# Performance work log

Measured on AMD Instinct MI355X. Metric: run time of the kernel, lower is better.

## Reference

```python
import jax, jax.numpy as jnp
import numpy as np

C = 5.0          # tanh clamp constant (args.c, non-trainable)
B, N, R, D = 4, 16, 64, 256  # batch, block_num, block_len, word_dim
NEG = -1e9


def setup_inputs() -> dict:
    key = jax.random.key(0)
    ks = iter(jax.random.split(key, 80))

    def W(i, o):
        # xavier-like init (torch stores (out,in); we store (in,out) and use x @ W)
        return jax.random.normal(next(ks), (i, o), jnp.float32) * np.float32(np.sqrt(2.0 / (i + o)))

    def bvec(d):
        return jax.random.normal(next(ks), (d,), jnp.float32) * 0.01

    inp = {"x": jax.random.normal(next(ks), (B, N, R, D), jnp.float32)}
    for p in ("fw", "bw"):
        inp[f"fcW_{p}"] = W(D, D);  inp[f"fcb_{p}"] = bvec(D)
        inp[f"mW1_{p}"] = W(D, D);  inp[f"mW2_{p}"] = W(D, D);  inp[f"mb_{p}"] = bvec(D)
        inp[f"s2tW1_{p}"] = W(D, D); inp[f"s2tb1_{p}"] = bvec(D)
        inp[f"s2tW_{p}"] = W(D, D);  inp[f"s2tb_{p}"] = bvec(D)
        inp[f"gW1_{p}"] = W(D, D);  inp[f"gW2_{p}"] = W(D, D);  inp[f"gb_{p}"] = bvec(D)
        inp[f"fW1_{p}"] = W(3 * D, D); inp[f"fb1_{p}"] = bvec(D)
        inp[f"fW2_{p}"] = W(3 * D, D); inp[f"fb2_{p}"] = bvec(D)
    return inp


def _mSA(x, W1, W2, b, fw):
    # x: (..., L, d) -> (..., L, d). Additive per-feature attention with strict
    # triangular mask. fw: token i attends to j > i (last row zeroed);
    # bw: token i attends to j < i (first row zeroed). Matches the torch
    # -inf mask + narrow + zero-pad construction exactly.
    L = x.shape[-2]
    xi = (x @ W1)[..., :, None, :]                 # (..., L, 1, d)
    xj = (x @ W2)[..., None, :, :]                 # (..., 1, L, d)
    f = C * jnp.tanh((xi + xj + b) / C)            # (..., i, j, d)
    i = jnp.arange(L)[:, None]
    j = jnp.arange(L)[None, :]
    allowed = (j > i) if fw else (j < i)           # (L, L)
    scores = jnp.where(allowed[..., None], f, NEG)
    att = jax.nn.softmax(scores, axis=-2)          # softmax over j
    rowvalid = (jnp.arange(L) < L - 1) if fw else (jnp.arange(L) > 0)
    att = att * rowvalid[:, None, None].astype(x.dtype)
    return jnp.einsum('...ijd,...jd->...id', att, x)


def _s2t(x, W1, b1, Wo, bo):
    # source2token self-attention: (..., L, d) -> (..., d)
    f = jax.nn.relu(x @ W1 + b1)
    a = jax.nn.softmax(f @ Wo + bo, axis=-2)
    return jnp.sum(a * x, axis=-2)


def _mblosa(x, mW1, mW2, mb, s2tW1, s2tb1, s2tW, s2tb,
            gW1, gW2, gb, fW1, fb1, fW2, fb2, fw):
    Bb, n, r, d = x.shape
    h = _mSA(x, mW1, mW2, mb, fw)                  # (B, n, r, d) intra-block
    v = _s2t(h, s2tW1, s2tb1, s2tW, s2tb)          # (B, n, d)    block summary
    o = _mSA(v, mW1, mW2, mb, fw)                  # (B, n, d)    inter-block
    G = jax.nn.sigmoid(o @ gW1 + v @ gW2 + gb)
    e = G * o + (1.0 - G) * v                      # (B, n, d)
    # torch: cat of e[i] repeated r times, then narrow(1, 0, n)
    idx = jnp.arange(n) // r
    E = e[:, idx]                                  # (B, n, d)
    # torch: flatten blocks then narrow(1, 0, n) (faithful to source)
    xf = x.reshape(Bb, n * r, d)[:, :n]
    hf = h.reshape(Bb, n * r, d)[:, :n]
    cat = jnp.concatenate([xf, hf, E], axis=-1)    # (B, n, 3d)
    fusion = jax.nn.relu(cat @ fW1 + fb1)
    Gf = jax.nn.sigmoid(cat @ fW2 + fb2)
    return Gf * fusion + (1.0 - Gf) * xf           # (B, n, d)


def reference(x,
              fcW_fw, fcb_fw, mW1_fw, mW2_fw, mb_fw, s2tW1_fw, s2tb1_fw,
              s2tW_fw, s2tb_fw, gW1_fw, gW2_fw, gb_fw, fW1_fw, fb1_fw,
              fW2_fw, fb2_fw,
              fcW_bw, fcb_bw, mW1_bw, mW2_bw, mb_bw, s2tW1_bw, s2tb1_bw,
              s2tW_bw, s2tb_bw, gW1_bw, gW2_bw, gb_bw, fW1_bw, fb1_bw,
              fW2_bw, fb2_bw):
    in_fw = jax.nn.relu(x @ fcW_fw + fcb_fw)
    in_bw = jax.nn.relu(x @ fcW_bw + fcb_bw)
    u_fw = _mblosa(in_fw, mW1_fw, mW2_fw, mb_fw, s2tW1_fw, s2tb1_fw,
                   s2tW_fw, s2tb_fw, gW1_fw, gW2_fw, gb_fw,
                   fW1_fw, fb1_fw, fW2_fw, fb2_fw, True)
    u_bw = _mblosa(in_bw, mW1_bw, mW2_bw, mb_bw, s2tW1_bw, s2tb1_bw,
                   s2tW_bw, s2tb_bw, gW1_bw, gW2_bw, gb_bw,
                   fW1_bw, fb1_bw, fW2_bw, fb2_bw, False)
    return jnp.concatenate([u_fw, u_bw], axis=-1)  # (B, n, 2d)
```

## Files before the change

### kernel.cpp

```cpp
#include <hip/hip_runtime.h>
#include <hip/hip_bf16.h>

typedef __hip_bfloat16 BF16;
typedef __attribute__((ext_vector_type(8))) short short8;
typedef __attribute__((ext_vector_type(4))) float f32x4;

#define MFMA_B16(a,b,c) __builtin_amdgcn_mfma_f32_16x16x32_bf16((a),(b),(c),0,0,0)

__device__ __forceinline__ short f2bs(float f){ BF16 h = __float2bfloat16(f); return *(short*)&h; }
__device__ __forceinline__ float bs2f(short s){ BF16 h = *(BF16*)&s; return __bfloat162float(h); }

struct SrcPack { const float* s[10]; };

__global__ __launch_bounds__(256) void transpose_k(SrcPack p, short* __restrict__ Oh,
                                                   short* __restrict__ Ol)
{
    __shared__ float s[64][65];
    const float* W = p.s[blockIdx.y];
    short* oh = Oh + (size_t)blockIdx.y * 65536;
    short* ol = Ol + (size_t)blockIdx.y * 65536;
    int tr = (blockIdx.x >> 2) * 64, tc = (blockIdx.x & 3) * 64;
    #pragma unroll
    for (int i = 0; i < 16; i++) {
        int e = threadIdx.x + i * 256;
        int r = e >> 6, c = e & 63;
        s[c][r] = W[(size_t)(tr + r) * 256 + tc + c];
    }
    __syncthreads();
    #pragma unroll
    for (int i = 0; i < 16; i++) {
        int e = threadIdx.x + i * 256;
        int c2 = e >> 6, r2 = e & 63;
        float v = s[c2][r2];
        short hi = f2bs(v);
        short lo = f2bs(v - bs2f(hi));
        size_t oi = (size_t)(tc + c2) * 256 + tr + r2;
        oh[oi] = hi;
        ol[oi] = lo;
    }
}

template<int AM, int OM, int RELU, int BS>
__device__ __forceinline__ void gemm_body(const void* __restrict__ A0,
    const void* __restrict__ Alo,
    const short* __restrict__ Wh, const short* __restrict__ Wl,
    const float* __restrict__ bias, void* __restrict__ O0, void* __restrict__ O1,
    int row0, int col0)
{
    constexpr int LDK = 72;
    __shared__ short sAh[64 * LDK];
    __shared__ short sAl[(AM == 0) ? 8 : 64 * LDK];
    __shared__ short sBh[64 * LDK];
    __shared__ short sBl[BS ? 8 : 64 * LDK];
    int tid = threadIdx.x;
    int w = tid >> 6, l = tid & 63;
    int m = l & 15, q = l >> 4;
    int sr = w * 16 + m;

    f32x4 acc[4];
    #pragma unroll
    for (int cf = 0; cf < 4; cf++) acc[cf] = (f32x4)(0.f);

    for (int kh = 0; kh < 4; kh++) {
        int kbase = kh * 64;
        #pragma unroll
        for (int i = 0; i < 2; i++) {
            int kl = q * 8 + 32 * i;
            size_t gofs = (size_t)(row0 + sr) * 256 + kbase + kl;
            if (AM == 1) {
                const float* src = (const float*)A0 + gofs;
                float4 f0 = *(const float4*)src;
                float4 f1 = *(const float4*)(src + 4);
                short8 vh, vl;
                float tmp[8] = {f0.x, f0.y, f0.z, f0.w, f1.x, f1.y, f1.z, f1.w};
                #pragma unroll
                for (int j = 0; j < 8; j++) {
                    vh[j] = f2bs(tmp[j]);
                    vl[j] = f2bs(tmp[j] - bs2f(vh[j]));
                }
                *(short8*)&sAh[sr * LDK + kl] = vh;
                *(short8*)&sAl[sr * LDK + kl] = vl;
            } else if (AM == 2) {
                *(short8*)&sAh[sr * LDK + kl] = *(const short8*)((const short*)A0 + gofs);
                *(short8*)&sAl[sr * LDK + kl] = *(const short8*)((const short*)Alo + gofs);
            } else {
                *(short8*)&sAh[sr * LDK + kl] = *(const short8*)((const short*)A0 + gofs);
            }
            size_t gofsB = (size_t)(col0 + sr) * 256 + kbase + kl;
            *(short8*)&sBh[sr * LDK + kl] = *(const short8*)(Wh + gofsB);
            if (!BS)
                *(short8*)&sBl[sr * LDK + kl] = *(const short8*)(Wl + gofsB);
        }
        __syncthreads();
        #pragma unroll
        for (int ch = 0; ch < 2; ch++) {
            int k = ch * 32 + q * 8;
            short8 ah = *(const short8*)&sAh[(w * 16 + m) * LDK + k];
            short8 al = (AM != 0) ? *(const short8*)&sAl[(w * 16 + m) * LDK + k] : ah;
            #pragma unroll
            for (int cf = 0; cf < 4; cf++) {
                short8 bh = *(const short8*)&sBh[(cf * 16 + m) * LDK + k];
                acc[cf] = MFMA_B16(ah, bh, acc[cf]);
                if (!BS) {
                    short8 bl = *(const short8*)&sBl[(cf * 16 + m) * LDK + k];
                    acc[cf] = MFMA_B16(ah, bl, acc[cf]);
                }
                if (AM != 0)
                    acc[cf] = MFMA_B16(al, bh, acc[cf]);
            }
        }
        __syncthreads();
    }
    #pragma unroll
    for (int cf = 0; cf < 4; cf++) {
        int col = col0 + cf * 16 + m;
        float bv = bias ? bias[col] : 0.f;
        #pragma unroll
        for (int r = 0; r < 4; r++) {
            int row = row0 + w * 16 + q * 4 + r;
            float v = acc[cf][r] + bv;
            if (RELU) v = fmaxf(v, 0.f);
            size_t oi = (size_t)row * 256 + col;
            if (OM == 0) {
                ((float*)O0)[oi] = v;
            } else if (OM == 1) {
                ((short*)O0)[oi] = f2bs(v);
            } else {
                short hi = f2bs(v);
                ((short*)O0)[oi] = hi;
                ((short*)O1)[oi] = f2bs(v - bs2f(hi));
            }
        }
    }
}

struct GDir { const void* A0; const void* Al; const short* Wh; const short* Wl;
              const float* bias; void* O0; void* O1; };

template<int AM, int OM, int RELU, int BS>
__global__ __launch_bounds__(256) void gemm_k(GDir p0, GDir p1)
{
    GDir p = blockIdx.z ? p1 : p0;
    gemm_body<AM, OM, RELU, BS>(p.A0, p.Al, p.Wh, p.Wl, p.bias, p.O0, p.O1,
                                blockIdx.x * 64, blockIdx.y * 64);
}

struct G2Dir { const float* A; const short* W1h; const short* W1l;
               const short* W2h; const short* W2l; const float* b2;
               float* C1; float* C2; };

__global__ __launch_bounds__(256) void gemm2s_k(G2Dir p0, G2Dir p1)
{
    G2Dir p = blockIdx.z ? p1 : p0;
    int y = blockIdx.y;
    const short* Wh = (y < 4) ? p.W1h : p.W2h;
    const short* Wl = (y < 4) ? p.W1l : p.W2l;
    void* C = (y < 4) ? (void*)p.C1 : (void*)p.C2;
    const float* bias = (y < 4) ? nullptr : p.b2;
    gemm_body<1, 0, 0, 0>(p.A, nullptr, Wh, Wl, bias, C, nullptr, 0, (y & 3) * 64);
}

struct MbloDir { const short* Ah; const short* Al;
                 const short* W1h; const short* W2h;
                 const float* mb; short* Hh; short* Hl; int fw; };

__global__ __launch_bounds__(512) void mblo_k(MbloDir p0, MbloDir p1)
{
    __shared__ char smraw[49152] __attribute__((aligned(16)));
    short* gAh  = (short*)smraw;
    short* gAl  = gAh + 4608;
    short* gB1h = gAh + 9216;
    short* gB2h = gAh + 13824;
    float* aP = (float*)smraw;
    float* aQ = aP + 4096;
    float* aX = aP + 8192;

    MbloDir p = blockIdx.z ? p1 : p0;
    int tid = threadIdx.x;
    int w = tid >> 6, l = tid & 63;
    int m = l & 15, q = l >> 4;
    int rh = w >> 1;
    int cb = (w & 1) * 2;
    int row0 = blockIdx.x * 64, d0 = blockIdx.y * 64;
    int srow = tid >> 3;
    int skl  = (tid & 7) * 8;

    f32x4 acc1[2], acc2[2];
    #pragma unroll
    for (int cf = 0; cf < 2; cf++) { acc1[cf] = (f32x4)(0.f); acc2[cf] = (f32x4)(0.f); }

    for (int kh = 0; kh < 4; kh++) {
        int kbase = kh * 64;
        size_t ga = (size_t)(row0 + srow) * 256 + kbase + skl;
        *(short8*)&gAh[srow * 72 + skl] = *(const short8*)(p.Ah + ga);
        *(short8*)&gAl[srow * 72 + skl] = *(const short8*)(p.Al + ga);
        size_t gb = (size_t)(d0 + srow) * 256 + kbase + skl;
        *(short8*)&gB1h[srow * 72 + skl] = *(const short8*)(p.W1h + gb);
        *(short8*)&gB2h[srow * 72 + skl] = *(const short8*)(p.W2h + gb);
        __syncthreads();
        #pragma unroll
        for (int ch = 0; ch < 2; ch++) {
            int k = ch * 32 + q * 8;
            short8 ah = *(const short8*)&gAh[(rh * 16 + m) * 72 + k];
            short8 al = *(const short8*)&gAl[(rh * 16 + m) * 72 + k];
            #pragma unroll
            for (int cf = 0; cf < 2; cf++) {
                int bofs = ((cb + cf) * 16 + m) * 72 + k;
                short8 b1 = *(const short8*)&gB1h[bofs];
                acc1[cf] = MFMA_B16(ah, b1, acc1[cf]);
                acc1[cf] = MFMA_B16(al, b1, acc1[cf]);
                short8 b2 = *(const short8*)&gB2h[bofs];
                acc2[cf] = MFMA_B16(ah, b2, acc2[cf]);
                acc2[cf] = MFMA_B16(al, b2, acc2[cf]);
            }
        }
        __syncthreads();
    }
    #pragma unroll
    for (int cf = 0; cf < 2; cf++) {
        int col = (cb + cf) * 16 + m;
        float mbv = p.mb[d0 + col];
        #pragma unroll
        for (int r = 0; r < 4; r++) {
            int row = rh * 16 + q * 4 + r;
            aP[row * 64 + col] = __expf(0.4f * acc1[cf][r]);
            aQ[row * 64 + col] = __expf(0.4f * (acc2[cf][r] + mbv));
        }
    }
    {
        size_t gx = (size_t)(row0 + srow) * 256 + d0 + skl;
        short8 xh = *(const short8*)(p.Ah + gx);
        short8 xl = *(const short8*)(p.Al + gx);
        #pragma unroll
        for (int t = 0; t < 8; t++)
            aX[srow * 64 + skl + t] = bs2f(xh[t]) + bs2f(xl[t]);
    }
    __syncthreads();
    #pragma unroll
    for (int t = 0; t < 8; t++) {
        int i = w + 8 * t;
        float P = aP[i * 64 + l];
        int js = p.fw ? (i + 1) : 0;
        int je = p.fw ? 64 : i;
        float den = 0.f, num = 0.f;
        for (int j = js; j < je; j++) {
            float u = P * aQ[j * 64 + l];
            float r = __builtin_amdgcn_rcpf(1.f + u);
            float wgt = __expf(-10.f * r);
            den += wgt;
            num += wgt * aX[j * 64 + l];
        }
        float out = (je > js) ? (num * __builtin_amdgcn_rcpf(den)) : 0.f;
        short hi = f2bs(out);
        size_t oi = (size_t)(row0 + i) * 256 + d0 + l;
        p.Hh[oi] = hi;
        p.Hl[oi] = f2bs(out - bs2f(hi));
    }
}

struct PoolDir { const short* T1; const short* Wh; const short* Wl; const float* bias;
                 const short* Hh; const short* Hl; float* V; };

__global__ __launch_bounds__(256) void s2t_pool_k(PoolDir p0, PoolDir p1)
{
    __shared__ char smraw[37888] __attribute__((aligned(16)));
    short* gAh = (short*)smraw;
    short* gBh = gAh + 4608;
    short* gBl = gAh + 9216;
    float* aL = (float*)smraw;
    float* aH = aL + 4352;
    float* rm = aL + 8704;
    float* rd = aL + 8960;
    float* rn = aL + 9216;

    PoolDir p = blockIdx.z ? p1 : p0;
    int tid = threadIdx.x;
    int w = tid >> 6, l = tid & 63;
    int m = l & 15, q = l >> 4;
    int sr = w * 16 + m;
    int row0 = blockIdx.x * 64, d0 = blockIdx.y * 64;

    f32x4 acc[4];
    #pragma unroll
    for (int cf = 0; cf < 4; cf++) acc[cf] = (f32x4)(0.f);

    for (int kh = 0; kh < 4; kh++) {
        int kbase = kh * 64;
        #pragma unroll
        for (int i = 0; i < 2; i++) {
            int kl = q * 8 + 32 * i;
            *(short8*)&gAh[sr * 72 + kl] =
                *(const short8*)(p.T1 + (size_t)(row0 + sr) * 256 + kbase + kl);
            size_t gb = (size_t)(d0 + sr) * 256 + kbase + kl;
            *(short8*)&gBh[sr * 72 + kl] = *(const short8*)(p.Wh + gb);
            *(short8*)&gBl[sr * 72 + kl] = *(const short8*)(p.Wl + gb);
        }
        __syncthreads();
        #pragma unroll
        for (int ch = 0; ch < 2; ch++) {
            int k = ch * 32 + q * 8;
            short8 ah = *(const short8*)&gAh[(w * 16 + m) * 72 + k];
            #pragma unroll
            for (int cf = 0; cf < 4; cf++) {
                int bofs = (cf * 16 + m) * 72 + k;
                short8 bh = *(const short8*)&gBh[bofs];
                short8 bl = *(const short8*)&gBl[bofs];
                acc[cf] = MFMA_B16(ah, bh, acc[cf]);
                acc[cf] = MFMA_B16(ah, bl, acc[cf]);
            }
        }
        __syncthreads();
    }
    #pragma unroll
    for (int cf = 0; cf < 4; cf++) {
        int col = cf * 16 + m;
        float bv = p.bias[d0 + col];
        #pragma unroll
        for (int r = 0; r < 4; r++) {
            int row = w * 16 + q * 4 + r;
            aL[row * 68 + col] = acc[cf][r] + bv;
        }
    }
    #pragma unroll
    for (int it = 0; it < 2; it++) {
        int e = tid + it * 256;
        int j = e >> 3, d8 = (e & 7) * 8;
        short8 xh = *(const short8*)(p.Hh + (size_t)(row0 + j) * 256 + d0 + d8);
        short8 xl = *(const short8*)(p.Hl + (size_t)(row0 + j) * 256 + d0 + d8);
        #pragma unroll
        for (int t = 0; t < 8; t++)
            aH[j * 68 + d8 + t] = bs2f(xh[t]) + bs2f(xl[t]);
    }
    __syncthreads();
    int dl = tid & 63, rq = tid >> 6;
    float mx = -1e30f, den = 0.f, num = 0.f;
    #pragma unroll
    for (int rr = 0; rr < 16; rr++) {
        int r = rq * 16 + rr;
        float lv = aL[r * 68 + dl];
        float hv = aH[r * 68 + dl];
        if (lv > mx) {
            float sc = __expf(mx - lv);
            den *= sc; num *= sc; mx = lv;
        }
        float wgt = __expf(lv - mx);
        den += wgt; num += wgt * hv;
    }
    rm[rq * 64 + dl] = mx; rd[rq * 64 + dl] = den; rn[rq * 64 + dl] = num;
    __syncthreads();
    if (rq == 0) {
        float M = fmaxf(fmaxf(rm[dl], rm[64 + dl]), fmaxf(rm[128 + dl], rm[192 + dl]));
        float D = 0.f, Nn = 0.f;
        #pragma unroll
        for (int k = 0; k < 4; k++) {
            float sc = __expf(rm[k * 64 + dl] - M);
            D += rd[k * 64 + dl] * sc;
            Nn += rn[k * 64 + dl] * sc;
        }
        p.V[(size_t)blockIdx.x * 256 + d0 + dl] = Nn / D;
    }
}

struct GateDir { const float* vW1; const float* vW2; const float* V;
                 const float* gW1; const float* gW2; const float* gb;
                 float* E0; int fw; };

__global__ __launch_bounds__(256) void attn2gate_k(GateDir p0, GateDir p1)
{
    GateDir p = blockIdx.z ? p1 : p0;
    __shared__ float so[256], sv[256], red[4][64];
    int b = blockIdx.x, k = threadIdx.x;
    float o = 0.f;
    if (p.fw) {
        float qv = p.vW1[(size_t)(b * 16) * 256 + k];
        float den = 0.f, num = 0.f;
        for (int j = 1; j < 16; j++) {
            float z = (qv + p.vW2[(size_t)(b * 16 + j) * 256 + k]) * 0.2f;
            float e2 = __expf(2.f * z);
            float t = 1.f - 2.f / (e2 + 1.f);
            float wgt = __expf(5.f * t);
            den += wgt; num += wgt * p.V[(size_t)(b * 16 + j) * 256 + k];
        }
        o = num / den;
    }
    so[k] = o;
    sv[k] = p.V[(size_t)(b * 16) * 256 + k];
    __syncthreads();
    int c = k & 63, ks = k >> 6;
    int gc = blockIdx.y * 64 + c;
    float acc = 0.f;
    int k0 = ks * 64;
    #pragma unroll 8
    for (int kk = 0; kk < 64; kk++) {
        int kx = k0 + kk;
        acc += so[kx] * p.gW1[(size_t)kx * 256 + gc] + sv[kx] * p.gW2[(size_t)kx * 256 + gc];
    }
    red[ks][c] = acc;
    __syncthreads();
    if (ks == 0) {
        float a = red[0][c] + red[1][c] + red[2][c] + red[3][c] + p.gb[gc];
        float G = 1.f / (1.f + __expf(-a));
        p.E0[b * 256 + gc] = G * so[gc] + (1.f - G) * sv[gc];
    }
}

struct FuseDir { const short* INh; const short* INl; const short* Hh; const short* Hl;
                 const float* E0; const float* fW1; const float* fb1;
                 const float* fW2; const float* fb2; };

__global__ __launch_bounds__(256) void fusion_k(FuseDir p0, FuseDir p1, float* __restrict__ out)
{
    FuseDir p = blockIdx.z ? p1 : p0;
    __shared__ float cat[768];
    __shared__ float red1[4][64], red2[4][64];
    int bt = blockIdx.x, b = bt >> 4, t = bt & 15;
    int c = threadIdx.x & 63, ks = threadIdx.x >> 6;
    int gc = blockIdx.y * 64 + c;
    size_t xrow = ((size_t)b * 1024 + t) * 256;
    cat[threadIdx.x]       = bs2f(p.INh[xrow + threadIdx.x]) + bs2f(p.INl[xrow + threadIdx.x]);
    cat[256 + threadIdx.x] = bs2f(p.Hh[xrow + threadIdx.x]) + bs2f(p.Hl[xrow + threadIdx.x]);
    cat[512 + threadIdx.x] = p.E0[b * 256 + threadIdx.x];
    __syncthreads();
    float a1 = 0.f, a2 = 0.f;
    int k0 = ks * 192;
    #pragma unroll 8
    for (int kk = 0; kk < 192; kk++) {
        int k = k0 + kk;
        float cv = cat[k];
        a1 += cv * p.fW1[(size_t)k * 256 + gc];
        a2 += cv * p.fW2[(size_t)k * 256 + gc];
    }
    red1[ks][c] = a1; red2[ks][c] = a2;
    __syncthreads();
    if (ks == 0) {
        float s1 = red1[0][c] + red1[1][c] + red1[2][c] + red1[3][c] + p.fb1[gc];
        float s2 = red2[0][c] + red2[1][c] + red2[2][c] + red2[3][c] + p.fb2[gc];
        float fus = fmaxf(s1, 0.f);
        float Gf = 1.f / (1.f + __expf(-s2));
        float u = Gf * fus + (1.f - Gf) * cat[gc];
        out[((size_t)(b * 16 + t)) * 512 + (size_t)blockIdx.z * 256 + gc] = u;
    }
}

extern "C" void kernel_launch(void* const* d_in, const int* in_sizes, int n_in,
                              void* d_out, int out_size, void* d_ws, size_t ws_size,
                              hipStream_t stream)
{
    const float* x = (const float*)d_in[0];
    char* base = (char*)d_ws;
    auto alloc = [&](size_t bytes){ void* r = base; base += (bytes + 255) & ~255ULL; return r; };
    short* inH = (short*)alloc(2 * 1048576 * 2);
    short* inL = (short*)alloc(2 * 1048576 * 2);
    short* hH  = (short*)alloc(2 * 1048576 * 2);
    short* hL  = (short*)alloc(2 * 1048576 * 2);
    short* t1  = (short*)alloc(2 * 1048576 * 2);
    short* wtH = (short*)alloc(10 * 65536 * 2);
    short* wtL = (short*)alloc(10 * 65536 * 2);
    float* v   = (float*)alloc(2 * 16384 * 4);
    float* vW1 = (float*)alloc(2 * 16384 * 4);
    float* vW2 = (float*)alloc(2 * 16384 * 4);
    float* E0  = (float*)alloc(2 * 1024 * 4);

    SrcPack sp;
    const int src_idx[5] = {0, 2, 3, 5, 7};
    for (int p = 0; p < 2; p++)
        for (int i = 0; i < 5; i++)
            sp.s[p * 5 + i] = (const float*)d_in[1 + p * 16 + src_idx[i]];
    transpose_k<<<dim3(16, 10), 256, 0, stream>>>(sp, wtH, wtL);

    GDir fc[2], s2t1[2];
    MbloDir mbd[2];
    PoolDir pld[2];
    G2Dir g2d[2];
    GateDir gtd[2];
    FuseDir fsd[2];
    for (int p = 0; p < 2; p++) {
        int bi = 1 + p * 16;
        const float* fcb   = (const float*)d_in[bi + 1];
        const float* mb    = (const float*)d_in[bi + 4];
        const float* s2tb1 = (const float*)d_in[bi + 6];
        const float* s2tb  = (const float*)d_in[bi + 8];
        size_t po = (size_t)p * 1048576;
        const short* W0h = wtH + (size_t)(p * 5 + 0) * 65536, *W0l = wtL + (size_t)(p * 5 + 0) * 65536;
        const short* W1h = wtH + (size_t)(p * 5 + 1) * 65536, *W1l = wtL + (size_t)(p * 5 + 1) * 65536;
        const short* W2h = wtH + (size_t)(p * 5 + 2) * 65536, *W2l = wtL + (size_t)(p * 5 + 2) * 65536;
        const short* W3h = wtH + (size_t)(p * 5 + 3) * 65536;
        const short* W4h = wtH + (size_t)(p * 5 + 4) * 65536, *W4l = wtL + (size_t)(p * 5 + 4) * 65536;

        fc[p]   = { x, nullptr, W0h, W0l, fcb, inH + po, inL + po };
        mbd[p]  = { inH + po, inL + po, W1h, W2h, mb, hH + po, hL + po, (p == 0) };
        s2t1[p] = { hH + po, hL + po, W3h, nullptr, s2tb1, t1 + po, nullptr };
        pld[p]  = { t1 + po, W4h, W4l, s2tb, hH + po, hL + po, v + p * 16384 };
        g2d[p]  = { v + p * 16384, W1h, W1l, W2h, W2l, mb, vW1 + p * 16384, vW2 + p * 16384 };
        gtd[p]  = { vW1 + p * 16384, vW2 + p * 16384, v + p * 16384,
                    (const float*)d_in[bi + 9], (const float*)d_in[bi + 10],
                    (const float*)d_in[bi + 11], E0 + p * 1024, (p == 0) };
        fsd[p]  = { inH + po, inL + po, hH + po, hL + po, E0 + p * 1024,
                    (const float*)d_in[bi + 12], (const float*)d_in[bi + 13],
                    (const float*)d_in[bi + 14], (const float*)d_in[bi + 15] };
    }

    gemm_k<1, 2, 1, 0><<<dim3(64, 4, 2), 256, 0, stream>>>(fc[0], fc[1]);
    mblo_k<<<dim3(64, 4, 2), 512, 0, stream>>>(mbd[0], mbd[1]);
    gemm_k<2, 1, 1, 1><<<dim3(64, 4, 2), 256, 0, stream>>>(s2t1[0], s2t1[1]);
    s2t_pool_k<<<dim3(64, 4, 2), 256, 0, stream>>>(pld[0], pld[1]);
    gemm2s_k<<<dim3(1, 8, 2), 256, 0, stream>>>(g2d[0], g2d[1]);
    attn2gate_k<<<dim3(4, 4, 2), 256, 0, stream>>>(gtd[0], gtd[1]);
    fusion_k<<<dim3(64, 4, 2), 256, 0, stream>>>(fsd[0], fsd[1], (float*)d_out);
}
```

Before: 211.9 us.

## Pre-split x to bf16 hi/lo, unroll masked attention loop, drop pool lo weights

The weight-transpose kernel now also splits the input x into bf16 hi/lo halves once, so the first FC GEMM reads pre-split bf16 instead of converting fp32 per tile. The mblo attention inner loop is restructured into 4-wide groups, with masking only on the boundary group, and the shared-memory row stride is padded to 66 to avoid bank conflicts. The s2t pool GEMM drops the low-part weight MFMA, trading some precision for half the MFMA and load work there.

After: 212.4 us. About the same (+0.2%).

```diff
diff --git a/kernel.cpp b/kernel.cpp
--- a/kernel.cpp
+++ b/kernel.cpp
@@ -3,6 +3,7 @@
 
 typedef __hip_bfloat16 BF16;
 typedef __attribute__((ext_vector_type(8))) short short8;
+typedef __attribute__((ext_vector_type(4))) short short4v;
 typedef __attribute__((ext_vector_type(4))) float f32x4;
 
 #define MFMA_B16(a,b,c) __builtin_amdgcn_mfma_f32_16x16x32_bf16((a),(b),(c),0,0,0)
@@ -12,31 +13,50 @@
 
 struct SrcPack { const float* s[10]; };
 
-__global__ __launch_bounds__(256) void transpose_k(SrcPack p, short* __restrict__ Oh,
-                                                   short* __restrict__ Ol)
-{
-    __shared__ float s[64][65];
-    const float* W = p.s[blockIdx.y];
-    short* oh = Oh + (size_t)blockIdx.y * 65536;
-    short* ol = Ol + (size_t)blockIdx.y * 65536;
-    int tr = (blockIdx.x >> 2) * 64, tc = (blockIdx.x & 3) * 64;
-    #pragma unroll
-    for (int i = 0; i < 16; i++) {
-        int e = threadIdx.x + i * 256;
-        int r = e >> 6, c = e & 63;
-        s[c][r] = W[(size_t)(tr + r) * 256 + tc + c];
-    }
-    __syncthreads();
-    #pragma unroll
-    for (int i = 0; i < 16; i++) {
-        int e = threadIdx.x + i * 256;
-        int c2 = e >> 6, r2 = e & 63;
-        float v = s[c2][r2];
-        short hi = f2bs(v);
-        short lo = f2bs(v - bs2f(hi));
-        size_t oi = (size_t)(tc + c2) * 256 + tr + r2;
-        oh[oi] = hi;
-        ol[oi] = lo;
+__global__ __launch_bounds__(256) void prep_k(SrcPack p, const float* __restrict__ xsrc,
+    short* __restrict__ Oh, short* __restrict__ Ol,
+    short* __restrict__ xH, short* __restrict__ xL)
+{
+    if (blockIdx.y < 10) {
+        __shared__ float s[64][65];
+        const float* W = p.s[blockIdx.y];
+        short* oh = Oh + (size_t)blockIdx.y * 65536;
+        short* ol = Ol + (size_t)blockIdx.y * 65536;
+        int tr = (blockIdx.x >> 2) * 64, tc = (blockIdx.x & 3) * 64;
+        #pragma unroll
+        for (int i = 0; i < 16; i++) {
+            int e = threadIdx.x + i * 256;
+            int r = e >> 6, c = e & 63;
+            s[c][r] = W[(size_t)(tr + r) * 256 + tc + c];
+        }
+        __syncthreads();
+        #pragma unroll
+        for (int i = 0; i < 16; i++) {
+            int e = threadIdx.x + i * 256;
+            int c2 = e >> 6, r2 = e & 63;
+            float v = s[c2][r2];
+            short hi = f2bs(v);
+            short lo = f2bs(v - bs2f(hi));
+            size_t oi = (size_t)(tc + c2) * 256 + tr + r2;
+            oh[oi] = hi;
+            ol[oi] = lo;
+        }
+    } else {
+        size_t base0 = (size_t)(blockIdx.y - 10) * 524288
+                     + (size_t)blockIdx.x * 32768 + threadIdx.x * 4;
+        for (int it = 0; it < 32; it++) {
+            size_t idx = base0 + (size_t)it * 1024;
+            float4 f = *(const float4*)&xsrc[idx];
+            float v[4] = {f.x, f.y, f.z, f.w};
+            short4v h, lo;
+            #pragma unroll
+            for (int t = 0; t < 4; t++) {
+                h[t] = f2bs(v[t]);
+                lo[t] = f2bs(v[t] - bs2f(h[t]));
+            }
+            *(short4v*)&xH[idx] = h;
+            *(short4v*)&xL[idx] = lo;
+        }
     }
 }
 
@@ -160,20 +180,39 @@
     gemm_body<1, 0, 0, 0>(p.A, nullptr, Wh, Wl, bias, C, nullptr, 0, (y & 3) * 64);
 }
 
+template<bool MASK>
+__device__ __forceinline__ void att_grp(const float* __restrict__ aQ,
+    const float* __restrict__ aX, int l, float P, int jb, int lo, int hi,
+    float& den, float& num)
+{
+    #pragma unroll
+    for (int u4 = 0; u4 < 4; u4++) {
+        int j = jb + u4;
+        float q = aQ[j * 66 + l];
+        float xv = aX[j * 66 + l];
+        float uu = P * q;
+        float r = __builtin_amdgcn_rcpf(1.f + uu);
+        float wgt = __expf(-10.f * r);
+        if (MASK) wgt = (j >= lo && j < hi) ? wgt : 0.f;
+        den += wgt;
+        num += wgt * xv;
+    }
+}
+
 struct MbloDir { const short* Ah; const short* Al;
                  const short* W1h; const short* W2h;
                  const float* mb; short* Hh; short* Hl; int fw; };
 
 __global__ __launch_bounds__(512) void mblo_k(MbloDir p0, MbloDir p1)
 {
-    __shared__ char smraw[49152] __attribute__((aligned(16)));
+    __shared__ char smraw[50688] __attribute__((aligned(16)));
     short* gAh  = (short*)smraw;
     short* gAl  = gAh + 4608;
     short* gB1h = gAh + 9216;
     short* gB2h = gAh + 13824;
     float* aP = (float*)smraw;
-    float* aQ = aP + 4096;
-    float* aX = aP + 8192;
+    float* aQ = aP + 4224;
+    float* aX = aP + 8448;
 
     MbloDir p = blockIdx.z ? p1 : p0;
     int tid = threadIdx.x;
@@ -223,8 +262,8 @@
         #pragma unroll
         for (int r = 0; r < 4; r++) {
             int row = rh * 16 + q * 4 + r;
-            aP[row * 64 + col] = __expf(0.4f * acc1[cf][r]);
-            aQ[row * 64 + col] = __expf(0.4f * (acc2[cf][r] + mbv));
+            aP[row * 66 + col] = __expf(0.4f * acc1[cf][r]);
+            aQ[row * 66 + col] = __expf(0.4f * (acc2[cf][r] + mbv));
         }
     }
     {
@@ -233,24 +272,32 @@
         short8 xl = *(const short8*)(p.Al + gx);
         #pragma unroll
         for (int t = 0; t < 8; t++)
-            aX[srow * 64 + skl + t] = bs2f(xh[t]) + bs2f(xl[t]);
-    }
-    __syncthreads();
-    #pragma unroll
+            aX[srow * 66 + skl + t] = bs2f(xh[t]) + bs2f(xl[t]);
+    }
+    __syncthreads();
     for (int t = 0; t < 8; t++) {
         int i = w + 8 * t;
-        float P = aP[i * 64 + l];
-        int js = p.fw ? (i + 1) : 0;
-        int je = p.fw ? 64 : i;
+        float P = aP[i * 66 + l];
         float den = 0.f, num = 0.f;
-        for (int j = js; j < je; j++) {
-            float u = P * aQ[j * 64 + l];
-            float r = __builtin_amdgcn_rcpf(1.f + u);
-            float wgt = __expf(-10.f * r);
-            den += wgt;
-            num += wgt * aX[j * 64 + l];
-        }
-        float out = (je > js) ? (num * __builtin_amdgcn_rcpf(den)) : 0.f;
+        bool valid;
+        if (p.fw) {
+            int js = i + 1;
+            int jb0 = js & ~3;
+            if (jb0 < 64)
+                att_grp<true>(aQ, aX, l, P, jb0, js, 64, den, num);
+            for (int jb = jb0 + 4; jb < 64; jb += 4)
+                att_grp<false>(aQ, aX, l, P, jb, 0, 64, den, num);
+            valid = (i < 63);
+        } else {
+            int je = i;
+            int jb1 = (je + 3) & ~3;
+            for (int jb = 0; jb + 4 < jb1; jb += 4)
+                att_grp<false>(aQ, aX, l, P, jb, 0, 64, den, num);
+            if (jb1 > 0)
+                att_grp<true>(aQ, aX, l, P, jb1 - 4, 0, je, den, num);
+            valid = (i > 0);
+        }
+        float out = valid ? (num * __builtin_amdgcn_rcpf(den)) : 0.f;
         short hi = f2bs(out);
         size_t oi = (size_t)(row0 + i) * 256 + d0 + l;
         p.Hh[oi] = hi;
@@ -258,7 +305,7 @@
     }
 }
 
-struct PoolDir { const short* T1; const short* Wh; const short* Wl; const float* bias;
+struct PoolDir { const short* T1; const short* Wh; const float* bias;
                  const short* Hh; const short* Hl; float* V; };
 
 __global__ __launch_bounds__(256) void s2t_pool_k(PoolDir p0, PoolDir p1)
@@ -266,7 +313,6 @@
     __shared__ char smraw[37888] __attribute__((aligned(16)));
     short* gAh = (short*)smraw;
     short* gBh = gAh + 4608;
-    short* gBl = gAh + 9216;
     float* aL = (float*)smraw;
     float* aH = aL + 4352;
     float* rm = aL + 8704;
@@ -291,9 +337,8 @@
             int kl = q * 8 + 32 * i;
             *(short8*)&gAh[sr * 72 + kl] =
                 *(const short8*)(p.T1 + (size_t)(row0 + sr) * 256 + kbase + kl);
-            size_t gb = (size_t)(d0 + sr) * 256 + kbase + kl;
-            *(short8*)&gBh[sr * 72 + kl] = *(const short8*)(p.Wh + gb);
-            *(short8*)&gBl[sr * 72 + kl] = *(const short8*)(p.Wl + gb);
+            *(short8*)&gBh[sr * 72 + kl] =
+                *(const short8*)(p.Wh + (size_t)(d0 + sr) * 256 + kbase + kl);
         }
         __syncthreads();
         #pragma unroll
@@ -302,11 +347,8 @@
             short8 ah = *(const short8*)&gAh[(w * 16 + m) * 72 + k];
             #pragma unroll
             for (int cf = 0; cf < 4; cf++) {
-                int bofs = (cf * 16 + m) * 72 + k;
-                short8 bh = *(const short8*)&gBh[bofs];
-                short8 bl = *(const short8*)&gBl[bofs];
+                short8 bh = *(const short8*)&gBh[(cf * 16 + m) * 72 + k];
                 acc[cf] = MFMA_B16(ah, bh, acc[cf]);
-                acc[cf] = MFMA_B16(ah, bl, acc[cf]);
             }
         }
         __syncthreads();
@@ -454,6 +496,8 @@
     short* hH  = (short*)alloc(2 * 1048576 * 2);
     short* hL  = (short*)alloc(2 * 1048576 * 2);
     short* t1  = (short*)alloc(2 * 1048576 * 2);
+    short* xH  = (short*)alloc(1048576 * 2);
+    short* xL  = (short*)alloc(1048576 * 2);
     short* wtH = (short*)alloc(10 * 65536 * 2);
     short* wtL = (short*)alloc(10 * 65536 * 2);
     float* v   = (float*)alloc(2 * 16384 * 4);
@@ -466,7 +510,7 @@
     for (int p = 0; p < 2; p++)
         for (int i = 0; i < 5; i++)
             sp.s[p * 5 + i] = (const float*)d_in[1 + p * 16 + src_idx[i]];
-    transpose_k<<<dim3(16, 10), 256, 0, stream>>>(sp, wtH, wtL);
+    prep_k<<<dim3(16, 12), 256, 0, stream>>>(sp, x, wtH, wtL, xH, xL);
 
     GDir fc[2], s2t1[2];
     MbloDir mbd[2];
@@ -485,12 +529,12 @@
         const short* W1h = wtH + (size_t)(p * 5 + 1) * 65536, *W1l = wtL + (size_t)(p * 5 + 1) * 65536;
         const short* W2h = wtH + (size_t)(p * 5 + 2) * 65536, *W2l = wtL + (size_t)(p * 5 + 2) * 65536;
         const short* W3h = wtH + (size_t)(p * 5 + 3) * 65536;
-        const short* W4h = wtH + (size_t)(p * 5 + 4) * 65536, *W4l = wtL + (size_t)(p * 5 + 4) * 65536;
-
-        fc[p]   = { x, nullptr, W0h, W0l, fcb, inH + po, inL + po };
+        const short* W4h = wtH + (size_t)(p * 5 + 4) * 65536;
+
+        fc[p]   = { xH, xL, W0h, W0l, fcb, inH + po, inL + po };
         mbd[p]  = { inH + po, inL + po, W1h, W2h, mb, hH + po, hL + po, (p == 0) };
         s2t1[p] = { hH + po, hL + po, W3h, nullptr, s2tb1, t1 + po, nullptr };
-        pld[p]  = { t1 + po, W4h, W4l, s2tb, hH + po, hL + po, v + p * 16384 };
+        pld[p]  = { t1 + po, W4h, s2tb, hH + po, hL + po, v + p * 16384 };
         g2d[p]  = { v + p * 16384, W1h, W1l, W2h, W2l, mb, vW1 + p * 16384, vW2 + p * 16384 };
         gtd[p]  = { vW1 + p * 16384, vW2 + p * 16384, v + p * 16384,
                     (const float*)d_in[bi + 9], (const float*)d_in[bi + 10],
@@ -500,7 +544,7 @@
                     (const float*)d_in[bi + 14], (const float*)d_in[bi + 15] };
     }
 
-    gemm_k<1, 2, 1, 0><<<dim3(64, 4, 2), 256, 0, stream>>>(fc[0], fc[1]);
+    gemm_k<2, 2, 1, 0><<<dim3(64, 4, 2), 256, 0, stream>>>(fc[0], fc[1]);
     mblo_k<<<dim3(64, 4, 2), 512, 0, stream>>>(mbd[0], mbd[1]);
     gemm_k<2, 1, 1, 1><<<dim3(64, 4, 2), 256, 0, stream>>>(s2t1[0], s2t1[1]);
     s2t_pool_k<<<dim3(64, 4, 2), 256, 0, stream>>>(pld[0], pld[1]);
```
